# Optimization experiments

Measured on AMD Instinct MI355X. Metric: run time of the kernel, lower is better.

The kernel has to match this reference:

```python
import jax, jax.numpy as jnp
import numpy as np

IN_CH = 64
OUT_CH = 64
SEQ_LEN = 2048
MODES = 64  # modes2 = min(modes1, seq_len//2) = 64
SCALE = 1.0 / (IN_CH * OUT_CH)


def setup_inputs() -> dict:
    key = jax.random.key(0)
    k1, k2, k3 = jax.random.split(key, 3)
    x = jax.random.normal(k1, (32, 8, IN_CH, SEQ_LEN), dtype=jnp.float32)
    # torch.rand(...) complex init scaled by 1/(in*out): real & imag in [0, scale)
    wr = SCALE * jax.random.uniform(k2, (IN_CH, OUT_CH, MODES), dtype=jnp.float32)
    wi = SCALE * jax.random.uniform(k3, (IN_CH, OUT_CH, MODES), dtype=jnp.float32)
    return {"x": x, "wr": wr, "wi": wi}


def reference(x, wr, wi):
    # x: [B, H, E, N] real; weights complex [in, out, modes]
    N = x.shape[-1]
    w = jax.lax.complex(wr, wi)
    x_ft = jnp.fft.rfft(x)                       # [B, H, E, N//2+1] complex64
    a = x_ft[..., :MODES]                        # keep only low modes
    out_low = jnp.einsum('bjix,iox->bjox', a, w)  # per-mode complex matmul
    # zero-fill remaining frequency bins (equivalent to out_ft zeros + slice set)
    pad = N // 2 + 1 - MODES
    out_ft = jnp.pad(out_low, ((0, 0), (0, 0), (0, 0), (0, pad)))
    return jnp.fft.irfft(out_ft, n=N)            # [B, H, out_ch, N] real
```

## Files before the change

kernel.cpp:

```cpp
#include <hip/hip_runtime.h>
#include <hip/hip_bf16.h>


typedef __bf16 bf16x8 __attribute__((ext_vector_type(8)));
typedef float  f32x4  __attribute__((ext_vector_type(4)));

#define SEQ 2048
#define NM2 128

__device__ __forceinline__ unsigned int rnbf(float f) {
  unsigned int u = __builtin_bit_cast(unsigned int, f);
  return (u + 0x7fffu + ((u >> 16) & 1u)) >> 16;
}
__device__ __forceinline__ unsigned int pack2(float a, float b) {
  return rnbf(a) | (rnbf(b) << 16);
}

typedef const __attribute__((address_space(1))) unsigned int gu32;
typedef __attribute__((address_space(3))) unsigned int lu32;

__global__ __launch_bounds__(256) void k_tables(unsigned short* __restrict__ t1sw,
                                                unsigned short* __restrict__ t2sw) {
  int idx = blockIdx.x * 256 + threadIdx.x;
  int k = idx >> 11;
  int n = idx & 2047;
  float rev = (float)((k * n) & 2047) * (1.0f / 2048.0f);
  float s, co;
  asm("v_sin_f32 %0, %1" : "=v"(s)  : "v"(rev));
  asm("v_cos_f32 %0, %1" : "=v"(co) : "v"(rev));
  float ck = (k == 0 ? 1.0f : 2.0f) * (1.0f / 2048.0f);
  {
    int kt = n >> 6, part = (n >> 3) & 7, e = n & 7;
    unsigned base = (unsigned)kt * 16384u + 2u * (unsigned)e;
    unsigned offc = base + (((unsigned)(k * 128 + part * 16)) ^ (((unsigned)k & 7u) << 4));
    int c2 = k + 64;
    unsigned offs = base + (((unsigned)(c2 * 128 + part * 16)) ^ (((unsigned)c2 & 7u) << 4));
    *(unsigned short*)((char*)t1sw + offc) = (unsigned short)rnbf(co);
    *(unsigned short*)((char*)t1sw + offs) = (unsigned short)rnbf(-s);
  }
  {
    int tile = n >> 7, rl = n & 127;
    unsigned rowbase = (unsigned)tile * 32768u + (unsigned)rl * 128u;
    unsigned kpart = ((((unsigned)(k >> 3)) * 16u) ^ (((unsigned)rl & 7u) << 4)) + 2u * ((unsigned)k & 7u);
    *(unsigned short*)((char*)t2sw + rowbase + kpart)          = (unsigned short)rnbf(ck * co);
    *(unsigned short*)((char*)t2sw + rowbase + 16384u + kpart) = (unsigned short)rnbf(-ck * s);
  }
}

__global__ __launch_bounds__(512) void k_gemm1f(const float* __restrict__ x,
                                                const unsigned short* __restrict__ t1sw,
                                                const float* __restrict__ wre,
                                                const float* __restrict__ wim,
                                                char* __restrict__ Bxsw) {
  __shared__ int4 lds4[65536 / 16];
  char* lds = (char*)lds4;
  const int tid = threadIdx.x, wave = tid >> 6, lane = tid & 63;
  const int bj = blockIdx.x;
  const int r0 = bj * 64;

  const float* xsrc[2];
#pragma unroll
  for (int p = 0; p < 2; ++p) {
    const int row = p * 32 + wave * 4 + (lane >> 4);
    const int u = (lane & 15) ^ (row & 7);
    xsrc[p] = x + (size_t)(r0 + row) * SEQ + u * 4;
  }

  f32x4 acc[4] = {};

#define XSTAGE(it, buf)                                                               \
  {                                                                                   \
    _Pragma("unroll")                                                                 \
    for (int p = 0; p < 2; ++p)                                                       \
      __builtin_amdgcn_global_load_lds((gu32*)(xsrc[p] + (it) * 64),                  \
          (lu32*)(lds + (buf) * 16384 + p * 8192 + wave * 1024), 16, 0, 0);           \
  }
#define TSTAGE(it, buf)                                                               \
  {                                                                                   \
    const char* tg_ = (const char*)t1sw + (size_t)(it) * 16384;                       \
    _Pragma("unroll")                                                                 \
    for (int q = 0; q < 2; ++q)                                                       \
      __builtin_amdgcn_global_load_lds((gu32*)(tg_ + (q * 512 + tid) * 16),           \
          (lu32*)(lds + 32768 + (buf) * 16384 + q * 8192 + wave * 1024), 16, 0, 0);   \
  }

  XSTAGE(0, 0);
  TSTAGE(0, 0);
  asm volatile("s_waitcnt vmcnt(0)" ::: "memory");
  __builtin_amdgcn_s_barrier();

  const int wr4 = wave >> 1, wc = wave & 1;
  const int a = wr4 * 16 + (lane & 15);
  const unsigned xra = (unsigned)(a & 7) << 4;
  const int kg = lane >> 4;

  for (int it = 0; it < 32; ++it) {
    const int cur = it & 1, nxt = cur ^ 1;
    const int xoff = cur * 16384;
    const int toff = 32768 + cur * 16384;
    if (it < 31) {
      XSTAGE(it + 1, nxt);
      TSTAGE(it + 1, nxt);
    }
#pragma unroll
    for (int kss = 0; kss < 2; ++kss) {
      const unsigned byte0 = (unsigned)(a * 256 + kss * 128 + kg * 32);
      const f32x4 lo = *(const f32x4*)(lds + xoff + (byte0 ^ xra));
      const f32x4 hi = *(const f32x4*)(lds + xoff + ((byte0 + 16) ^ xra));
      unsigned c0, c1, c2, c3;
      asm("v_cvt_pk_bf16_f32 %0, %1, %2" : "=v"(c0) : "v"(lo[0]), "v"(lo[1]));
      asm("v_cvt_pk_bf16_f32 %0, %1, %2" : "=v"(c1) : "v"(lo[2]), "v"(lo[3]));
      asm("v_cvt_pk_bf16_f32 %0, %1, %2" : "=v"(c2) : "v"(hi[0]), "v"(hi[1]));
      asm("v_cvt_pk_bf16_f32 %0, %1, %2" : "=v"(c3) : "v"(hi[2]), "v"(hi[3]));
      uint4 pk; pk.x = c0; pk.y = c1; pk.z = c2; pk.w = c3;
      const bf16x8 av = __builtin_bit_cast(bf16x8, pk);
#pragma unroll
      for (int t = 0; t < 4; ++t) {
        const int col = wc * 64 + t * 16 + (lane & 15);
        const bf16x8 bv = *(const bf16x8*)(lds + toff +
            ((col * 128 + kss * 64 + kg * 16) ^ ((unsigned)(col & 7) << 4)));
        acc[t] = __builtin_amdgcn_mfma_f32_16x16x32_bf16(bv, av, acc[t], 0, 0, 0);
      }
    }
    asm volatile("s_waitcnt vmcnt(0)" ::: "memory");
    __builtin_amdgcn_s_barrier();
  }
#undef XSTAGE
#undef TSTAGE

  float* sA = (float*)lds;
#pragma unroll
  for (int t = 0; t < 4; ++t) {
    const int col0 = wc * 64 + t * 16 + kg * 4;
    *(f32x4*)(sA + a * 136 + col0) = acc[t];
  }
  __syncthreads();

  const int o = tid >> 3;
  const int kb = (tid & 7) * 8;
  f32x4 accr0 = {}, accr1 = {}, acci0 = {}, acci1 = {};
  for (int i = 0; i < 64; ++i) {
    const float* wp = wre + (size_t)(i * 64 + o) * 64 + kb;
    const float* wq = wim + (size_t)(i * 64 + o) * 64 + kb;
    const f32x4 w0 = *(const f32x4*)(wp),     w1 = *(const f32x4*)(wp + 4);
    const f32x4 v0 = *(const f32x4*)(wq),     v1 = *(const f32x4*)(wq + 4);
    const float* ap = sA + i * 136 + kb;
    const f32x4 ar0 = *(const f32x4*)(ap),      ar1 = *(const f32x4*)(ap + 4);
    const f32x4 ai0 = *(const f32x4*)(ap + 64), ai1 = *(const f32x4*)(ap + 68);
#pragma unroll
    for (int kk = 0; kk < 4; ++kk) {
      accr0[kk] += ar0[kk] * w0[kk] - ai0[kk] * v0[kk];
      accr1[kk] += ar1[kk] * w1[kk] - ai1[kk] * v1[kk];
      acci0[kk] += ar0[kk] * v0[kk] + ai0[kk] * w0[kk];
      acci1[kk] += ar1[kk] * v1[kk] + ai1[kk] * w1[kk];
    }
  }
  const int r = bj * 64 + o;
  const int tile = r >> 7, rl = r & 127;
  char* bb = Bxsw + (size_t)tile * 32768 + (size_t)rl * 128;
  const unsigned kp0 = (((unsigned)(kb >> 3)) * 16u) ^ (((unsigned)rl & 7u) << 4);
  uint4 vr; vr.x = pack2(accr0[0], accr0[1]); vr.y = pack2(accr0[2], accr0[3]);
            vr.z = pack2(accr1[0], accr1[1]); vr.w = pack2(accr1[2], accr1[3]);
  uint4 vi; vi.x = pack2(acci0[0], acci0[1]); vi.y = pack2(acci0[2], acci0[3]);
            vi.z = pack2(acci1[0], acci1[1]); vi.w = pack2(acci1[2], acci1[3]);
  *(uint4*)(bb + kp0)         = vr;
  *(uint4*)(bb + 16384 + kp0) = vi;
}

__global__ __launch_bounds__(256) void k_gemm2(const char* __restrict__ Bxsw,
                                               const char* __restrict__ t2sw,
                                               float* __restrict__ out) {
  __shared__ int4 lds4[49152 / 16];
  char* lds = (char*)lds4;
  const int tid = threadIdx.x, wave = tid >> 6, lane = tid & 63;
  const int swz = (blockIdx.x & 7) * 512 + (blockIdx.x >> 3);
  const int mb = swz >> 5, nb64 = swz & 31;
  const int r0 = mb * 128, n0 = nb64 * 64;
  const char* bsrc = Bxsw + (size_t)mb * 32768;
  const char* tsrc = t2sw + (size_t)(nb64 >> 1) * 32768 + (size_t)(nb64 & 1) * 8192;
#pragma unroll
  for (int i = 0; i < 4; ++i)
    __builtin_amdgcn_global_load_lds((gu32*)(bsrc + i * 4096 + tid * 16),
                                     (lu32*)(lds + i * 4096 + wave * 1024), 16, 0, 0);
#pragma unroll
  for (int i = 0; i < 2; ++i)
    __builtin_amdgcn_global_load_lds((gu32*)(tsrc + i * 4096 + tid * 16),
                                     (lu32*)(lds + 32768 + i * 4096 + wave * 1024), 16, 0, 0);
#pragma unroll
  for (int i = 0; i < 4; ++i)
    __builtin_amdgcn_global_load_lds((gu32*)(bsrc + 16384 + i * 4096 + tid * 16),
                                     (lu32*)(lds + 16384 + i * 4096 + wave * 1024), 16, 0, 0);
#pragma unroll
  for (int i = 0; i < 2; ++i)
    __builtin_amdgcn_global_load_lds((gu32*)(tsrc + 16384 + i * 4096 + tid * 16),
                                     (lu32*)(lds + 40960 + i * 4096 + wave * 1024), 16, 0, 0);
  asm volatile("s_waitcnt vmcnt(6)" ::: "memory");
  __builtin_amdgcn_s_barrier();

  f32x4 acc[2][4] = {};
  const int rowA0 = wave * 32 + (lane & 15);
  const int rowA1 = rowA0 + 16;
  const unsigned xa0 = (unsigned)(rowA0 & 7) << 4;
  const unsigned xa1 = (unsigned)(rowA1 & 7) << 4;

#pragma unroll
  for (int half = 0; half < 2; ++half) {
    if (half == 1) {
      asm volatile("s_waitcnt vmcnt(0)" ::: "memory");
      __builtin_amdgcn_s_barrier();
    }
    const int ab = half * 16384;
    const int bb = 32768 + half * 8192;
#pragma unroll
    for (int kq = 0; kq < 2; ++kq) {
      const unsigned offh = (unsigned)(kq * 64 + (lane >> 4) * 16);
      const bf16x8 a0 = *(const bf16x8*)(lds + ab + rowA0 * 128 + (offh ^ xa0));
      const bf16x8 a1 = *(const bf16x8*)(lds + ab + rowA1 * 128 + (offh ^ xa1));
#pragma unroll
      for (int t = 0; t < 4; ++t) {
        const int rn = t * 16 + (lane & 15);
        const bf16x8 bv = *(const bf16x8*)(lds + bb + rn * 128 + (offh ^ ((unsigned)(rn & 7) << 4)));
        acc[0][t] = __builtin_amdgcn_mfma_f32_16x16x32_bf16(a0, bv, acc[0][t], 0, 0, 0);
        acc[1][t] = __builtin_amdgcn_mfma_f32_16x16x32_bf16(a1, bv, acc[1][t], 0, 0, 0);
      }
    }
  }
#pragma unroll
  for (int m = 0; m < 2; ++m) {
#pragma unroll
    for (int j = 0; j < 4; ++j) {
      const int row = r0 + wave * 32 + m * 16 + (lane >> 4) * 4 + j;
#pragma unroll
      for (int t = 0; t < 4; ++t) {
        const int col = n0 + t * 16 + (lane & 15);
        out[(size_t)row * SEQ + col] = acc[m][t][j];
      }
    }
  }
}

extern "C" void kernel_launch(void* const* d_in, const int* in_sizes, int n_in,
                              void* d_out, int out_size, void* d_ws, size_t ws_size,
                              hipStream_t stream) {
  const float* x  = (const float*)d_in[0];
  const float* wr = (const float*)d_in[1];
  const float* wi = (const float*)d_in[2];
  float* out = (float*)d_out;
  char* ws = (char*)d_ws;
  unsigned short* t1sw = (unsigned short*)(ws);
  unsigned short* t2sw = (unsigned short*)(ws + 524288);
  char*           Bxsw = (char*)(ws + 1048576);

  k_tables<<<dim3(512),  dim3(256), 0, stream>>>(t1sw, t2sw);
  k_gemm1f<<<dim3(256),  dim3(512), 0, stream>>>(x, t1sw, wr, wi, Bxsw);
  k_gemm2 <<<dim3(4096), dim3(256), 0, stream>>>(Bxsw, (const char*)t2sw, out);
}
```

Baseline: 89.76 us.

## Split gemm1 mode columns across two blocks to double grid parallelism

The forward DFT GEMM kernel now launches 512 blocks of 256 threads instead of 256 blocks of 512, and each block handles half the modes (32 cos plus 32 sin columns) for its 64 rows. The table staging gathers only the needed columns, and the per-mode complex weight contraction is also split by mode half. The aim is better CU occupancy, since 256 blocks underfill the 256 CUs once multiple blocks per CU are possible, and lower LDS per block. The cost is that each x tile is loaded and converted twice, doubling x reads from global memory.

```diff
diff --git a/kernel.cpp b/kernel.cpp
--- a/kernel.cpp
+++ b/kernel.cpp
@@ -47,23 +47,31 @@
   }
 }
 
-__global__ __launch_bounds__(512) void k_gemm1f(const float* __restrict__ x,
+__global__ __launch_bounds__(256) void k_gemm1f(const float* __restrict__ x,
                                                 const unsigned short* __restrict__ t1sw,
                                                 const float* __restrict__ wre,
                                                 const float* __restrict__ wim,
                                                 char* __restrict__ Bxsw) {
-  __shared__ int4 lds4[65536 / 16];
+  __shared__ int4 lds4[49152 / 16];
   char* lds = (char*)lds4;
   const int tid = threadIdx.x, wave = tid >> 6, lane = tid & 63;
-  const int bj = blockIdx.x;
+  const int bj = blockIdx.x >> 1, kh = blockIdx.x & 1;
   const int r0 = bj * 64;
 
-  const float* xsrc[2];
-#pragma unroll
-  for (int p = 0; p < 2; ++p) {
-    const int row = p * 32 + wave * 4 + (lane >> 4);
+  const float* xsrc[4];
+#pragma unroll
+  for (int p = 0; p < 4; ++p) {
+    const int row = p * 16 + wave * 4 + (lane >> 4);
     const int u = (lane & 15) ^ (row & 7);
     xsrc[p] = x + (size_t)(r0 + row) * SEQ + u * 4;
+  }
+  const char* t1src[2];
+#pragma unroll
+  for (int q = 0; q < 2; ++q) {
+    const int l = q * 256 + tid;
+    const int rl = l >> 3, part = l & 7;
+    const int c = kh * 32 + (rl & 31) + ((rl & 32) << 1);
+    t1src[q] = (const char*)t1sw + c * 128 + part * 16;
   }
 
   f32x4 acc[4] = {};
@@ -71,17 +79,16 @@
 #define XSTAGE(it, buf)                                                               \
   {                                                                                   \
     _Pragma("unroll")                                                                 \
-    for (int p = 0; p < 2; ++p)                                                       \
+    for (int p = 0; p < 4; ++p)                                                       \
       __builtin_amdgcn_global_load_lds((gu32*)(xsrc[p] + (it) * 64),                  \
-          (lu32*)(lds + (buf) * 16384 + p * 8192 + wave * 1024), 16, 0, 0);           \
+          (lu32*)(lds + (buf) * 16384 + p * 4096 + wave * 1024), 16, 0, 0);           \
   }
 #define TSTAGE(it, buf)                                                               \
   {                                                                                   \
-    const char* tg_ = (const char*)t1sw + (size_t)(it) * 16384;                       \
     _Pragma("unroll")                                                                 \
     for (int q = 0; q < 2; ++q)                                                       \
-      __builtin_amdgcn_global_load_lds((gu32*)(tg_ + (q * 512 + tid) * 16),           \
-          (lu32*)(lds + 32768 + (buf) * 16384 + q * 8192 + wave * 1024), 16, 0, 0);   \
+      __builtin_amdgcn_global_load_lds((gu32*)(t1src[q] + (size_t)(it) * 16384),      \
+          (lu32*)(lds + 32768 + (buf) * 8192 + q * 4096 + wave * 1024), 16, 0, 0);    \
   }
 
   XSTAGE(0, 0);
@@ -89,15 +96,14 @@
   asm volatile("s_waitcnt vmcnt(0)" ::: "memory");
   __builtin_amdgcn_s_barrier();
 
-  const int wr4 = wave >> 1, wc = wave & 1;
-  const int a = wr4 * 16 + (lane & 15);
+  const int a = wave * 16 + (lane & 15);
   const unsigned xra = (unsigned)(a & 7) << 4;
   const int kg = lane >> 4;
 
   for (int it = 0; it < 32; ++it) {
     const int cur = it & 1, nxt = cur ^ 1;
     const int xoff = cur * 16384;
-    const int toff = 32768 + cur * 16384;
+    const int toff = 32768 + cur * 8192;
     if (it < 31) {
       XSTAGE(it + 1, nxt);
       TSTAGE(it + 1, nxt);
@@ -116,9 +122,9 @@
       const bf16x8 av = __builtin_bit_cast(bf16x8, pk);
 #pragma unroll
       for (int t = 0; t < 4; ++t) {
-        const int col = wc * 64 + t * 16 + (lane & 15);
+        const int lc = t * 16 + (lane & 15);
         const bf16x8 bv = *(const bf16x8*)(lds + toff +
-            ((col * 128 + kss * 64 + kg * 16) ^ ((unsigned)(col & 7) << 4)));
+            ((lc * 128 + kss * 64 + kg * 16) ^ ((unsigned)(lc & 7) << 4)));
         acc[t] = __builtin_amdgcn_mfma_f32_16x16x32_bf16(bv, av, acc[t], 0, 0, 0);
       }
     }
@@ -131,22 +137,23 @@
   float* sA = (float*)lds;
 #pragma unroll
   for (int t = 0; t < 4; ++t) {
-    const int col0 = wc * 64 + t * 16 + kg * 4;
-    *(f32x4*)(sA + a * 136 + col0) = acc[t];
+    const int lc0 = t * 16 + kg * 4;
+    *(f32x4*)(sA + a * 68 + lc0) = acc[t];
   }
   __syncthreads();
 
-  const int o = tid >> 3;
-  const int kb = (tid & 7) * 8;
+  const int o = tid >> 2;
+  const int jb = (tid & 3) * 8;
+  const int kglo = kh * 32 + jb;
   f32x4 accr0 = {}, accr1 = {}, acci0 = {}, acci1 = {};
   for (int i = 0; i < 64; ++i) {
-    const float* wp = wre + (size_t)(i * 64 + o) * 64 + kb;
-    const float* wq = wim + (size_t)(i * 64 + o) * 64 + kb;
-    const f32x4 w0 = *(const f32x4*)(wp),     w1 = *(const f32x4*)(wp + 4);
-    const f32x4 v0 = *(const f32x4*)(wq),     v1 = *(const f32x4*)(wq + 4);
-    const float* ap = sA + i * 136 + kb;
+    const float* wp = wre + (size_t)(i * 64 + o) * 64 + kglo;
+    const float* wq = wim + (size_t)(i * 64 + o) * 64 + kglo;
+    const f32x4 w0 = *(const f32x4*)(wp),      w1 = *(const f32x4*)(wp + 4);
+    const f32x4 v0 = *(const f32x4*)(wq),      v1 = *(const f32x4*)(wq + 4);
+    const float* ap = sA + i * 68 + jb;
     const f32x4 ar0 = *(const f32x4*)(ap),      ar1 = *(const f32x4*)(ap + 4);
-    const f32x4 ai0 = *(const f32x4*)(ap + 64), ai1 = *(const f32x4*)(ap + 68);
+    const f32x4 ai0 = *(const f32x4*)(ap + 32), ai1 = *(const f32x4*)(ap + 36);
 #pragma unroll
     for (int kk = 0; kk < 4; ++kk) {
       accr0[kk] += ar0[kk] * w0[kk] - ai0[kk] * v0[kk];
@@ -158,7 +165,7 @@
   const int r = bj * 64 + o;
   const int tile = r >> 7, rl = r & 127;
   char* bb = Bxsw + (size_t)tile * 32768 + (size_t)rl * 128;
-  const unsigned kp0 = (((unsigned)(kb >> 3)) * 16u) ^ (((unsigned)rl & 7u) << 4);
+  const unsigned kp0 = (((unsigned)(kglo >> 3)) * 16u) ^ (((unsigned)rl & 7u) << 4);
   uint4 vr; vr.x = pack2(accr0[0], accr0[1]); vr.y = pack2(accr0[2], accr0[3]);
             vr.z = pack2(accr1[0], accr1[1]); vr.w = pack2(accr1[2], accr1[3]);
   uint4 vi; vi.x = pack2(acci0[0], acci0[1]); vi.y = pack2(acci0[2], acci0[3]);
@@ -252,6 +259,6 @@
   char*           Bxsw = (char*)(ws + 1048576);
 
   k_tables<<<dim3(512),  dim3(256), 0, stream>>>(t1sw, t2sw);
-  k_gemm1f<<<dim3(256),  dim3(512), 0, stream>>>(x, t1sw, wr, wi, Bxsw);
+  k_gemm1f<<<dim3(512),  dim3(256), 0, stream>>>(x, t1sw, wr, wi, Bxsw);
   k_gemm2 <<<dim3(4096), dim3(256), 0, stream>>>(Bxsw, (const char*)t2sw, out);
 }
```

Result: slower. 117.7 us (+31.2%).
